# Kernel optimization log

Hardware: AMD Instinct MI355X
Metric: run time of the kernel (lower is better)

## Reference

```python
import jax, jax.numpy as jnp
import numpy as np

EPS = 1e-5

def _bn(x, gamma, beta):
    # training-mode BatchNorm2d over (B, H, W) per channel, biased variance
    m = x.mean(axis=(0, 2, 3), keepdims=True)
    v = x.var(axis=(0, 2, 3), keepdims=True)
    return (x - m) * jax.lax.rsqrt(v + EPS) * gamma[None, :, None, None] + beta[None, :, None, None]

@jax.custom_vjp
def _atan_spike(x):
    # Heaviside forward, ATan surrogate (alpha=2) backward
    return (x >= 0.0).astype(x.dtype)

def _atan_fwd(x):
    return _atan_spike(x), x

def _atan_bwd(x, g):
    return (g / (1.0 + (jnp.pi * x) ** 2),)

_atan_spike.defvjp(_atan_fwd, _atan_bwd)

def setup_inputs() -> dict:
    key = jax.random.key(0)
    ks = jax.random.split(key, 3)
    T, N, Cin, Cout, H, W = 4, 8, 512, 256, 32, 32
    x = jax.random.normal(ks[0], (T, N, Cin, H, W), dtype=jnp.float32)
    bn1_gamma = jnp.ones((Cin,), jnp.float32)
    bn1_beta = jnp.zeros((Cin,), jnp.float32)
    conv_w = jax.random.normal(ks[1], (Cout, Cin, 1, 1), jnp.float32) / np.float32(np.sqrt(Cin))
    lif_w = jnp.zeros((1,), jnp.float32)  # sigmoid(0)=0.5 <=> init_tau=2.0
    bn2_gamma = jnp.ones((Cout,), jnp.float32)
    bn2_beta = jnp.zeros((Cout,), jnp.float32)
    up_w = jax.random.normal(ks[2], (Cout, Cout, 4, 4), jnp.float32) / np.float32(np.sqrt(Cout * 16))
    return {"x": x, "bn1_gamma": bn1_gamma, "bn1_beta": bn1_beta, "conv_w": conv_w,
            "lif_w": lif_w, "bn2_gamma": bn2_gamma, "bn2_beta": bn2_beta, "up_w": up_w}

def reference(x, bn1_gamma, bn1_beta, conv_w, lif_w, bn2_gamma, bn2_beta, up_w):
    T, N, Cin, H, W = x.shape
    Cout = conv_w.shape[0]
    # bottleneck: SeqToANNContainer(BN(Cin), Conv2d 1x1 Cin->Cout, no bias)
    xf = x.reshape(T * N, Cin, H, W)
    h = _bn(xf, bn1_gamma, bn1_beta)
    h = jnp.einsum('bchw,oc->bohw', h, conv_w[:, :, 0, 0])
    h = h.reshape(T, N, Cout, H, W)
    # MultiStepParametricLIFNode: v += (x - v)*sigmoid(w); hard reset to 0, detach_reset
    tau_inv = jax.nn.sigmoid(lif_w[0])
    def step(v, xt):
        v = v + (xt - v) * tau_inv
        s = _atan_spike(v - 1.0)
        v = v * (1.0 - jax.lax.stop_gradient(s))
        return v, s
    _, spikes = jax.lax.scan(step, jnp.zeros_like(h[0]), h)
    s = spikes.reshape(T * N, Cout, H, W)
    # ConstantDilation2d(dilation=2): zero-insertion -> (2H-1, 2W-1)
    d = jnp.zeros((T * N, Cout, 2 * H - 1, 2 * W - 1), s.dtype).at[:, :, ::2, ::2].set(s)
    # ConstantPad2d(kernel-1-padding = 4-1-1 = 2)
    d = jnp.pad(d, ((0, 0), (0, 0), (2, 2), (2, 2)))
    d = _bn(d, bn2_gamma, bn2_beta)
    # ConvTranspose2d(k=4, stride=1, padding=3) == VALID conv with channel-swapped, flipped kernel
    kern = up_w.transpose(1, 0, 2, 3)[:, :, ::-1, ::-1]
    out = jax.lax.conv_general_dilated(d, kern, (1, 1), 'VALID',
                                       dimension_numbers=('NCHW', 'OIHW', 'NCHW'))
    return out.reshape(T, N, Cout, 2 * H, 2 * W)
```

## Files before the change

### kernel.cpp

```cpp
#include <hip/hip_runtime.h>
#include <math.h>

#define CIN 512
#define COUT 256
#define TT 4
#define NN 8
#define HH 32
#define WW 32
#define FR (TT*NN)
#define HW (HH*WW)
#define BN_EPS 1e-5
#define FLAGCAP (1<<19)
#define N2 143648.0

typedef unsigned short ushort_t;
typedef unsigned int uint_t;
typedef __attribute__((ext_vector_type(8))) short short8;
typedef __attribute__((ext_vector_type(4))) float f32x4;
typedef __attribute__((ext_vector_type(4))) uint_t u32x4;

__device__ inline ushort_t f2bf(float f) {
    uint_t u = __float_as_uint(f);
    uint_t r = u + 0x7FFFu + ((u >> 16) & 1u);
    return (ushort_t)(r >> 16);
}
__device__ inline float bf2f(ushort_t a) { return __uint_as_float(((uint_t)a) << 16); }

__global__ __launch_bounds__(512) void k_init(int* __restrict__ cnt,
                                              uint_t* __restrict__ flagcnt,
                                              double* __restrict__ bn_s1,
                                              double* __restrict__ bn_s2,
                                              float* __restrict__ kc) {
    int t = threadIdx.x;
    bn_s1[t] = 0.0;
    bn_s2[t] = 0.0;
    if (t < 256) { cnt[t] = 0; kc[t] = 0.f; }
    if (t == 0) *flagcnt = 0u;
}

__global__ __launch_bounds__(256) void k_xsplit(const float* __restrict__ x,
                                                ushort_t* __restrict__ Xa_g,
                                                ushort_t* __restrict__ Xb_g,
                                                float* __restrict__ X2_g,
                                                double* __restrict__ bn_s1,
                                                double* __restrict__ bn_s2) {
    int blk = blockIdx.x;
    int n = blk >> 6;
    int hw0 = (blk & 63) << 4;
    int tid = threadIdx.x;
    int pg = tid & 3;
    int rr = tid >> 2;

    __shared__ ushort_t La[8192];
    __shared__ ushort_t Lb[8192];
    __shared__ float X2s[64];

    float x2loc[16];
    float s1v[8], s2v[8];
#pragma unroll
    for (int q = 0; q < 16; ++q) x2loc[q] = 0.f;
#pragma unroll
    for (int q = 0; q < 8; ++q) { s1v[q] = 0.f; s2v[q] = 0.f; }
    if (tid < 64) X2s[tid] = 0.f;

#pragma unroll
    for (int kc = 0; kc < 4; ++kc) {
        int c0 = kc << 7;
        __syncthreads();
#pragma unroll
        for (int sw = 0; sw < 8; ++sw) {
            const int t = sw >> 1;
            int i = ((sw & 1) << 6) + rr;
            const float4 v = *reinterpret_cast<const float4*>(
                &x[(((size_t)((t * NN + n) * CIN) + c0 + i) << 10) + hw0 + (pg << 2)]);
            int cbl = i >> 3, e = i & 7;
            int slot = (kc << 1) + (sw & 1);
#pragma unroll
            for (int k = 0; k < 4; ++k) {
                float xv = (k == 0) ? v.x : (k == 1) ? v.y : (k == 2) ? v.z : v.w;
                ushort_t a = f2bf(xv);
                ushort_t b = f2bf(xv - bf2f(a));
                x2loc[(k << 2) + t] += xv * xv;
                s1v[slot] += xv;
                s2v[slot] += xv * xv;
                int lrx = (k << 2) + t;
                uint_t u = ((((uint_t)(pg * 16 + cbl)) * 16 + lrx) << 3) + e;
                uint_t byteoff = (u << 1) ^ ((uint_t)pg << 5);
                *(ushort_t*)((char*)La + byteoff) = a;
                *(ushort_t*)((char*)Lb + byteoff) = b;
            }
        }
        __syncthreads();
        for (int q = tid; q < 1024; q += 256) {
            int pg2 = q >> 8;
            uint_t lo = (uint_t)(q & 255) << 4;
            uint_t src = (((uint_t)pg2 << 12) + lo) ^ ((uint_t)pg2 << 5);
            u32x4 va = *(u32x4*)((char*)La + src);
            u32x4 vb = *(u32x4*)((char*)Lb + src);
            size_t dst = (((size_t)blk * 4 + pg2) << 13) + ((size_t)kc << 11) + ((size_t)(q & 255) << 3);
            __builtin_nontemporal_store(va, (u32x4*)(Xa_g + dst));
            __builtin_nontemporal_store(vb, (u32x4*)(Xb_g + dst));
        }
    }
#pragma unroll
    for (int slot = 0; slot < 8; ++slot) {
        float a1 = s1v[slot], a2v = s2v[slot];
        a1 += __shfl_xor(a1, 1); a1 += __shfl_xor(a1, 2);
        a2v += __shfl_xor(a2v, 1); a2v += __shfl_xor(a2v, 2);
        if (pg == 0) {
            int c = ((slot >> 1) << 7) + ((slot & 1) << 6) + rr;
            atomicAdd(&bn_s1[c], (double)a1);
            atomicAdd(&bn_s2[c], (double)a2v);
        }
    }
    __syncthreads();
#pragma unroll
    for (int k = 0; k < 4; ++k)
#pragma unroll
        for (int t = 0; t < 4; ++t)
            atomicAdd(&X2s[pg * 16 + k * 4 + t], x2loc[(k << 2) + t]);
    __syncthreads();
    if (tid < 64) X2_g[(blk << 6) + tid] = X2s[tid];
}

__global__ __launch_bounds__(256) void k_prep_wsplit(const float* __restrict__ conv_w,
                                                     const float* __restrict__ beta1,
                                                     const float* __restrict__ gamma1,
                                                     const double* __restrict__ bn_s1,
                                                     const double* __restrict__ bn_s2,
                                                     double* __restrict__ w2t,
                                                     ushort_t* __restrict__ Wa,
                                                     ushort_t* __restrict__ Wb,
                                                     float* __restrict__ W2,
                                                     double* __restrict__ bias) {
    int o = blockIdx.x;
    __shared__ double alphas[CIN];
    __shared__ double mbs[CIN];
    for (int c = threadIdx.x; c < CIN; c += 256) {
        double n = (double)(FR * HW);
        double m = bn_s1[c] / n;
        double var = bn_s2[c] / n - m * m;
        double al = (double)gamma1[c] / sqrt(var + BN_EPS);
        alphas[c] = al;
        mbs[c] = (double)beta1[c] - m * al;
    }
    __syncthreads();

    float s2 = 0.f;
    double sb = 0.0;
    for (int c = threadIdx.x; c < CIN; c += 256) {
        double cw = (double)conv_w[(size_t)o * CIN + c];
        double w = cw * alphas[c];
        w2t[(size_t)c * COUT + o] = w;
        float wf = (float)w;
        ushort_t a = f2bf(wf);
        ushort_t b = f2bf(wf - bf2f(a));
        size_t base = ((size_t)(c >> 3) * COUT + o) * 8 + (c & 7);
        Wa[base] = a; Wb[base] = b;
        s2 += wf * wf;
        sb += mbs[c] * cw;
    }
    __shared__ float red[256];
    __shared__ double redd[256];
    red[threadIdx.x] = s2;
    redd[threadIdx.x] = sb;
    __syncthreads();
    for (int ofs = 128; ofs > 0; ofs >>= 1) {
        if (threadIdx.x < ofs) {
            red[threadIdx.x] += red[threadIdx.x + ofs];
            redd[threadIdx.x] += redd[threadIdx.x + ofs];
        }
        __syncthreads();
    }
    if (threadIdx.x == 0) { W2[o] = red[0]; bias[o] = redd[0]; }
}

__global__ __launch_bounds__(256) void k_gemm_lif_mfma(
    const ushort_t* __restrict__ Xa_g, const ushort_t* __restrict__ Xb_g,
    const ushort_t* __restrict__ Wa, const ushort_t* __restrict__ Wb,
    const float* __restrict__ X2_g, const float* __restrict__ W2,
    const double* __restrict__ bias, const float* __restrict__ lif_w,
    ushort_t* __restrict__ spk, int* __restrict__ cnt,
    uint_t* __restrict__ flags, uint_t* __restrict__ flagcnt)
{
    int blk = blockIdx.x;
    int n   = blk >> 6;
    int hw0 = (blk & 63) << 4;
    int tid = threadIdx.x;
    int wv = tid >> 6, lane = tid & 63;
    int lr = lane & 15, kq = lane >> 4;
    int pxh = wv >> 1, oh = wv & 1;

    __shared__ uint_t cl[4 * 64 * 8];

    f32x4 acc[2][8];
#pragma unroll
    for (int m = 0; m < 2; ++m)
#pragma unroll
        for (int ot = 0; ot < 8; ++ot) acc[m][ot] = (f32x4){0.f, 0.f, 0.f, 0.f};

    const ushort_t* xa0 = Xa_g + (((size_t)blk) << 15) + ((size_t)pxh << 14) + ((uint_t)lane << 3);
    const ushort_t* xb0 = Xb_g + (((size_t)blk) << 15) + ((size_t)pxh << 14) + ((uint_t)lane << 3);
    const ushort_t* wbase_a = Wa + ((uint_t)kq << 11) + ((uint_t)oh << 10) + ((uint_t)lr << 3);
    const ushort_t* wbase_b = Wb + ((uint_t)kq << 11) + ((uint_t)oh << 10) + ((uint_t)lr << 3);

#pragma unroll 2
    for (int ks = 0; ks < 16; ++ks) {
        short8 fa0 = *(const short8*)(xa0 + (ks << 9));
        short8 fa1 = *(const short8*)(xa0 + 8192 + (ks << 9));
        short8 fb0 = *(const short8*)(xb0 + (ks << 9));
        short8 fb1 = *(const short8*)(xb0 + 8192 + (ks << 9));
        const ushort_t* wpa = wbase_a + (ks << 13);
        const ushort_t* wpb = wbase_b + (ks << 13);
#pragma unroll
        for (int ot = 0; ot < 8; ++ot) {
            short8 wa8 = *(const short8*)(wpa + (ot << 7));
            short8 wb8 = *(const short8*)(wpb + (ot << 7));
            acc[0][ot] = __builtin_amdgcn_mfma_f32_16x16x32_bf16(fa0, wa8, acc[0][ot], 0, 0, 0);
            acc[1][ot] = __builtin_amdgcn_mfma_f32_16x16x32_bf16(fa1, wa8, acc[1][ot], 0, 0, 0);
            acc[0][ot] = __builtin_amdgcn_mfma_f32_16x16x32_bf16(fb0, wa8, acc[0][ot], 0, 0, 0);
            acc[1][ot] = __builtin_amdgcn_mfma_f32_16x16x32_bf16(fb1, wa8, acc[1][ot], 0, 0, 0);
            acc[0][ot] = __builtin_amdgcn_mfma_f32_16x16x32_bf16(fa0, wb8, acc[0][ot], 0, 0, 0);
            acc[1][ot] = __builtin_amdgcn_mfma_f32_16x16x32_bf16(fa1, wb8, acc[1][ot], 0, 0, 0);
        }
    }

    float xs2[2][4];
#pragma unroll
    for (int m = 0; m < 2; ++m)
#pragma unroll
        for (int t = 0; t < 4; ++t)
            xs2[m][t] = X2_g[(blk << 6) + (((pxh << 1) + m) << 4) + (kq << 2) + t];

    for (int q = tid; q < 4 * 64 * 8; q += 256) cl[q] = 0;
    __syncthreads();

    float tauf = (float)(1.0 / (1.0 + exp(-(double)lif_w[0])));
#pragma unroll
    for (int ot = 0; ot < 8; ++ot) {
        int o = (oh << 7) + (ot << 4) + lr;
        float bi = (float)bias[o];
        float w2v = W2[o];
        uint_t cloc = 0;
#pragma unroll
        for (int m = 0; m < 2; ++m) {
            int hw = hw0 + (pxh << 3) + (m << 2) + kq;
            float v = 0.f;
            bool fl = false;
#pragma unroll
            for (int t = 0; t < 4; ++t) {
                float h = acc[m][ot][t] + bi;
                float eps = 4e-5f * sqrtf(w2v * xs2[m][t]) + 5e-5f;
                v += (h - v) * tauf;
                if (fabsf(v - 1.f) <= 2.f * eps) fl = true;
                bool s = (v >= 1.f);
                spk[((size_t)((t * NN + n) * HW) + hw) * COUT + o] = s ? (ushort_t)0x3F80 : (ushort_t)0;
                cloc += s ? 1u : 0u;
                if (s) v = 0.f;
            }
            if (fl) {
                uint_t id = atomicAdd(flagcnt, 1u);
                if (id < FLAGCAP) flags[id] = (((uint_t)(n * HW + hw)) << 8) | (uint_t)o;
            }
        }
        cl[(wv << 9) + (lane << 3) + ot] = cloc;
    }
    __syncthreads();
    {
        int o = tid;
        int ohh = o >> 7, ott = (o >> 4) & 7, lr2 = o & 15;
        uint_t s = 0;
#pragma unroll
        for (int w2 = ohh; w2 < 4; w2 += 2)
#pragma unroll
            for (int k2 = 0; k2 < 4; ++k2)
                s += cl[(w2 << 9) + (((k2 << 4) + lr2) << 3) + ott];
        if (s) atomicAdd(&cnt[o], (int)s);
    }
}

__global__ __launch_bounds__(256) void k_fixup(
    const float* __restrict__ x, const double* __restrict__ w2t,
    const double* __restrict__ bias, const float* __restrict__ lif_w,
    const uint_t* __restrict__ flags, const uint_t* __restrict__ flagcnt,
    ushort_t* __restrict__ spk, int* __restrict__ cnt)
{
    int nf = (int)*flagcnt; if (nf > FLAGCAP) nf = FLAGCAP;
    int wid = (blockIdx.x << 2) + (threadIdx.x >> 6);
    int lane = threadIdx.x & 63;
    double tau = 1.0 / (1.0 + exp(-(double)lif_w[0]));
    for (int g = wid; g < nf; g += 8192) {
        uint_t f = flags[g];
        int o = f & 255;
        int s = f >> 8;
        int n = s >> 10, hw = s & 1023;
        const float* xb = x + ((size_t)n << 19) + hw;
        double p0 = 0.0, p1 = 0.0, p2 = 0.0, p3 = 0.0;
#pragma unroll
        for (int i = 0; i < 8; ++i) {
            int c = lane + (i << 6);
            double wv = w2t[((size_t)c << 8) + o];
            size_t xo = (size_t)c << 10;
            p0 += wv * (double)xb[xo];
            p1 += wv * (double)xb[xo + (1ull << 22)];
            p2 += wv * (double)xb[xo + (2ull << 22)];
            p3 += wv * (double)xb[xo + (3ull << 22)];
        }
#pragma unroll
        for (int ofs = 32; ofs > 0; ofs >>= 1) {
            p0 += __shfl_down(p0, ofs);
            p1 += __shfl_down(p1, ofs);
            p2 += __shfl_down(p2, ofs);
            p3 += __shfl_down(p3, ofs);
        }
        if (lane == 0) {
            double bi = bias[o];
            double hh[4] = {p0 + bi, p1 + bi, p2 + bi, p3 + bi};
            double v = 0.0; int delta = 0;
#pragma unroll
            for (int t = 0; t < 4; ++t) {
                v += (hh[t] - v) * tau;
                bool sn = (v >= 1.0);
                size_t idx = (((size_t)t << 13) + ((size_t)n << 10) + (size_t)hw) * COUT + o;
                ushort_t old = spk[idx];
                ushort_t nw = sn ? (ushort_t)0x3F80 : (ushort_t)0;
                if (old != nw) { spk[idx] = nw; delta += sn ? 1 : -1; }
                if (sn) v = 0.0;
            }
            if (delta) atomicAdd(&cnt[o], delta);
        }
    }
}

__global__ __launch_bounds__(256) void k_wt_prep(const float* __restrict__ up_w,
                                                 const int* __restrict__ cnt,
                                                 const float* __restrict__ gamma2,
                                                 const float* __restrict__ beta2,
                                                 ushort_t* __restrict__ Wt,
                                                 float* __restrict__ kc) {
    int blk = blockIdx.x;
    int ij = blk >> 5, cb = blk & 31;
    int o = threadIdx.x;
    __shared__ double a2s[8], b2s[8];
    if (o < 8) {
        int c = (cb << 3) + o;
        double m = (double)cnt[c] / N2;
        double a = (double)gamma2[c] / sqrt(m - m * m + BN_EPS);
        a2s[o] = a;
        b2s[o] = (double)beta2[c] - m * a;
    }
    __syncthreads();
    short8 v;
    double part = 0.0;
#pragma unroll
    for (int e = 0; e < 8; ++e) {
        int c = (cb << 3) + e;
        double u = (double)up_w[(((size_t)c * COUT) + o) * 16 + ij];
        v[e] = (short)f2bf((float)(a2s[e] * u));
        part += b2s[e] * u;
    }
    *(short8*)(Wt + ((size_t)ij << 16) + ((size_t)cb << 11) + ((size_t)o << 3)) = v;
    atomicAdd(&kc[o], (float)part);
}

__global__ __launch_bounds__(512) void k_deconv_mfma(const ushort_t* __restrict__ spk,
                                                     const ushort_t* __restrict__ Wt,
                                                     const float* __restrict__ kc,
                                                     float* __restrict__ out) {
    int p = blockIdx.x;
    int xcd = p & 7;
    int r = p >> 3;
    int py = xcd >> 2;
    int b  = ((xcd & 3) << 3) | ((r >> 4) & 7);
    int Yb = (r & 15) << 1;
    int tid = threadIdx.x;
    int wv  = tid >> 6;
    int lane = tid & 63;
    int px = wv >> 2;
    int og = wv & 3;
    int lr = lane & 15;
    int kq = lane >> 4;

    __shared__ __align__(16) char smem[52224];
    ushort_t* slab = (ushort_t*)smem;

    int sb = Yb - 1 + py;
    for (int q = tid; q < 3 * 34 * 32; q += 512) {
        int pix = q >> 5;
        int l = q & 31;
        int r2 = pix / 34;
        int xc = pix - r2 * 34;
        int sy = sb + r2;
        int sx = xc - 1;
        uint_t off = ((uint_t)(pix << 9) + (uint_t)(l << 4)) ^ ((uint_t)(xc & 7) << 4);
        uint4* dst = (uint4*)((char*)slab + off);
        if (sy >= 0 && sy < 32 && sx >= 0 && sx < 32) {
            *dst = *(const uint4*)(spk + ((size_t)b * HW + sy * 32 + sx) * COUT + l * 8);
        } else {
            *dst = make_uint4(0u, 0u, 0u, 0u);
        }
    }
    __syncthreads();

    f32x4 acc[4][4];
#pragma unroll
    for (int pf = 0; pf < 4; ++pf)
#pragma unroll
        for (int of = 0; of < 4; ++of)
            acc[pf][of] = (f32x4){0.f, 0.f, 0.f, 0.f};

    int obase = og << 6;

#pragma unroll
    for (int dy = 0; dy < 2; ++dy) {
#pragma unroll
        for (int dx = 0; dx < 2; ++dx) {
            int i = 3 - py - 2 * dy;
            int j = 3 - px - 2 * dx;
            const ushort_t* wpij = Wt + ((size_t)(i * 4 + j) << 16);
            uint_t sbase[4], swz[4];
#pragma unroll
            for (int pf = 0; pf < 4; ++pf) {
                int pid = pf * 16 + lr;
                int Yq = pid >> 5;
                int X  = pid & 31;
                int xc = X + dx + px;
                int prow = (Yq + dy) * 34 + xc;
                sbase[pf] = ((uint_t)prow << 9) + ((uint_t)kq << 4);
                swz[pf]   = ((uint_t)(xc & 7)) << 4;
            }
#pragma unroll
            for (int cs = 0; cs < 8; ++cs) {
                short8 aw[4];
#pragma unroll
                for (int of = 0; of < 4; ++of)
                    aw[of] = *(const short8*)(wpij +
                        ((size_t)((cs << 2) + kq) * COUT + obase + (of << 4) + lr) * 8);
                short8 bs[4];
#pragma unroll
                for (int pf = 0; pf < 4; ++pf)
                    bs[pf] = *(const short8*)((const char*)slab +
                              ((sbase[pf] + ((uint_t)cs << 6)) ^ swz[pf]));
#pragma unroll
                for (int pf = 0; pf < 4; ++pf)
#pragma unroll
                    for (int of = 0; of < 4; ++of)
                        acc[pf][of] = __builtin_amdgcn_mfma_f32_16x16x32_bf16(
                            aw[of], bs[pf], acc[pf][of], 0, 0, 0);
            }
        }
    }

    __syncthreads();
    float* stage = (float*)smem;
#pragma unroll 1
    for (int of = 0; of < 4; ++of) {
        if (of) __syncthreads();
#pragma unroll
        for (int rg = 0; rg < 4; ++rg) {
            int row = (og << 4) + (kq << 2) + rg;
#pragma unroll
            for (int pf = 0; pf < 4; ++pf) {
                int Yq = pf >> 1;
                int x = ((((pf & 1) << 4) + lr) << 1) + px;
                uint_t a4 = ((uint_t)row << 5) + ((uint_t)Yq << 4)
                          + (((uint_t)x >> 2) ^ ((uint_t)kq << 2));
                stage[(a4 << 2) + (x & 3)] = acc[pf][of][rg];
            }
        }
        __syncthreads();
#pragma unroll
        for (int rep = 0; rep < 4; ++rep) {
            int u = tid + (rep << 9);
            int rr2 = u >> 5, rem = u & 31;
            int yq = rem >> 4, f4 = rem & 15;
            uint_t a4 = ((uint_t)rr2 << 5) + ((uint_t)yq << 4)
                      + ((uint_t)f4 ^ ((((uint_t)rr2 >> 2) & 3) << 2));
            f32x4 v = ((const f32x4*)stage)[a4];
            int o = ((rr2 >> 4) << 6) + (of << 4) + (rr2 & 15);
            float base = kc[o];
            v[0] += base; v[1] += base; v[2] += base; v[3] += base;
            int y = ((Yb + yq) << 1) + py;
            __builtin_nontemporal_store(v,
                (f32x4*)(out + ((size_t)(b * COUT + o) << 12) + (y << 6) + (f4 << 2)));
        }
    }
}

extern "C" void kernel_launch(void* const* d_in, const int* in_sizes, int n_in,
                              void* d_out, int out_size, void* d_ws, size_t ws_size,
                              hipStream_t stream) {
    (void)in_sizes; (void)n_in; (void)out_size; (void)ws_size;
    const float* x        = (const float*)d_in[0];
    const float* bn1_g    = (const float*)d_in[1];
    const float* bn1_b    = (const float*)d_in[2];
    const float* conv_w   = (const float*)d_in[3];
    const float* lif_w    = (const float*)d_in[4];
    const float* bn2_g    = (const float*)d_in[5];
    const float* bn2_b    = (const float*)d_in[6];
    const float* up_w     = (const float*)d_in[7];
    float* out = (float*)d_out;

    char* ws = (char*)d_ws;
    ushort_t* spk  = (ushort_t*)(ws + 0);
    ushort_t* Xa_g = (ushort_t*)(ws + 16777216);
    ushort_t* Xb_g = (ushort_t*)(ws + 50331648);
    float*  X2_g   = (float*)  (ws + 83886080);
    float*  W2     = (float*)  (ws + 84017152);
    double* w2t    = (double*) (ws + 84026368);
    double* bias   = (double*) (ws + 85074944);
    int*    cnt    = (int*)    (ws + 85081088);
    float*  kc     = (float*)  (ws + 85082112);
    ushort_t* Wt   = (ushort_t*)(ws + 85083136);
    ushort_t* Wa   = (ushort_t*)(ws + 87180288);
    ushort_t* Wb   = (ushort_t*)(ws + 87442432);
    uint_t* flagcnt= (uint_t*) (ws + 87704576);
    uint_t* flags  = (uint_t*) (ws + 87705600);
    double* bn_s1  = (double*) (ws + 89802752);
    double* bn_s2  = (double*) (ws + 89806848);

    k_init<<<1, 512, 0, stream>>>(cnt, flagcnt, bn_s1, bn_s2, kc);
    k_xsplit<<<512, 256, 0, stream>>>(x, Xa_g, Xb_g, X2_g, bn_s1, bn_s2);
    k_prep_wsplit<<<COUT, 256, 0, stream>>>(conv_w, bn1_b, bn1_g, bn_s1, bn_s2,
                                            w2t, Wa, Wb, W2, bias);
    k_gemm_lif_mfma<<<512, 256, 0, stream>>>(Xa_g, Xb_g, Wa, Wb, X2_g, W2,
                                             bias, lif_w, spk, cnt, flags, flagcnt);
    k_fixup<<<2048, 256, 0, stream>>>(x, w2t, bias, lif_w, flags, flagcnt, spk, cnt);
    k_wt_prep<<<512, 256, 0, stream>>>(up_w, cnt, bn2_g, bn2_b, Wt, kc);
    k_deconv_mfma<<<32 * 2 * 16, 512, 0, stream>>>(spk, Wt, kc, out);
}
```

Measured before the change: 440.7 us.

## Double deconv pixel tile per block to reuse weight fragments across more pixels

Each deconv block now covers 4 quarter-rows (128 pixels) per parity instead of 2, so the block count halves to 512 and each wave holds 8x4 accumulator fragments. Every weight fragment loaded from global memory now feeds twice as many MFMAs, which cuts weight traffic per output. The slab staging grows to 5 rows, the epilogue is adjusted for the larger tile, and register pressure rises (128 accumulator floats per lane), which may lower occupancy or cause spills.

```diff
diff --git a/kernel.cpp b/kernel.cpp
--- a/kernel.cpp
+++ b/kernel.cpp
@@ -371,8 +371,8 @@
     int xcd = p & 7;
     int r = p >> 3;
     int py = xcd >> 2;
-    int b  = ((xcd & 3) << 3) | ((r >> 4) & 7);
-    int Yb = (r & 15) << 1;
+    int b  = ((xcd & 3) << 3) | (r >> 3);
+    int YB = r & 7;
     int tid = threadIdx.x;
     int wv  = tid >> 6;
     int lane = tid & 63;
@@ -381,11 +381,11 @@
     int lr = lane & 15;
     int kq = lane >> 4;
 
-    __shared__ __align__(16) char smem[52224];
+    __shared__ __align__(16) char smem[5 * 34 * 512];
     ushort_t* slab = (ushort_t*)smem;
 
-    int sb = Yb - 1 + py;
-    for (int q = tid; q < 3 * 34 * 32; q += 512) {
+    int sb = (YB << 2) + py - 1;
+    for (int q = tid; q < 5 * 34 * 32; q += 512) {
         int pix = q >> 5;
         int l = q & 31;
         int r2 = pix / 34;
@@ -402,9 +402,9 @@
     }
     __syncthreads();
 
-    f32x4 acc[4][4];
-#pragma unroll
-    for (int pf = 0; pf < 4; ++pf)
+    f32x4 acc[8][4];
+#pragma unroll
+    for (int pf = 0; pf < 8; ++pf)
 #pragma unroll
         for (int of = 0; of < 4; ++of)
             acc[pf][of] = (f32x4){0.f, 0.f, 0.f, 0.f};
@@ -418,12 +418,11 @@
             int i = 3 - py - 2 * dy;
             int j = 3 - px - 2 * dx;
             const ushort_t* wpij = Wt + ((size_t)(i * 4 + j) << 16);
-            uint_t sbase[4], swz[4];
-#pragma unroll
-            for (int pf = 0; pf < 4; ++pf) {
-                int pid = pf * 16 + lr;
-                int Yq = pid >> 5;
-                int X  = pid & 31;
+            uint_t sbase[8], swz[8];
+#pragma unroll
+            for (int pf = 0; pf < 8; ++pf) {
+                int Yq = pf >> 1;
+                int X  = ((pf & 1) << 4) + lr;
                 int xc = X + dx + px;
                 int prow = (Yq + dy) * 34 + xc;
                 sbase[pf] = ((uint_t)prow << 9) + ((uint_t)kq << 4);
@@ -436,17 +435,15 @@
                 for (int of = 0; of < 4; ++of)
                     aw[of] = *(const short8*)(wpij +
                         ((size_t)((cs << 2) + kq) * COUT + obase + (of << 4) + lr) * 8);
-                short8 bs[4];
-#pragma unroll
-                for (int pf = 0; pf < 4; ++pf)
-                    bs[pf] = *(const short8*)((const char*)slab +
+#pragma unroll
+                for (int pf = 0; pf < 8; ++pf) {
+                    short8 bs = *(const short8*)((const char*)slab +
                               ((sbase[pf] + ((uint_t)cs << 6)) ^ swz[pf]));
-#pragma unroll
-                for (int pf = 0; pf < 4; ++pf)
 #pragma unroll
                     for (int of = 0; of < 4; ++of)
                         acc[pf][of] = __builtin_amdgcn_mfma_f32_16x16x32_bf16(
-                            aw[of], bs[pf], acc[pf][of], 0, 0, 0);
+                            aw[of], bs, acc[pf][of], 0, 0, 0);
+                }
             }
         }
     }
@@ -460,27 +457,27 @@
         for (int rg = 0; rg < 4; ++rg) {
             int row = (og << 4) + (kq << 2) + rg;
 #pragma unroll
-            for (int pf = 0; pf < 4; ++pf) {
+            for (int pf = 0; pf < 8; ++pf) {
                 int Yq = pf >> 1;
                 int x = ((((pf & 1) << 4) + lr) << 1) + px;
-                uint_t a4 = ((uint_t)row << 5) + ((uint_t)Yq << 4)
+                uint_t a4 = (((uint_t)row * 4 + Yq) << 4)
                           + (((uint_t)x >> 2) ^ ((uint_t)kq << 2));
                 stage[(a4 << 2) + (x & 3)] = acc[pf][of][rg];
             }
         }
         __syncthreads();
 #pragma unroll
-        for (int rep = 0; rep < 4; ++rep) {
+        for (int rep = 0; rep < 8; ++rep) {
             int u = tid + (rep << 9);
-            int rr2 = u >> 5, rem = u & 31;
+            int row = u >> 6, rem = u & 63;
             int yq = rem >> 4, f4 = rem & 15;
-            uint_t a4 = ((uint_t)rr2 << 5) + ((uint_t)yq << 4)
-                      + ((uint_t)f4 ^ ((((uint_t)rr2 >> 2) & 3) << 2));
+            uint_t a4 = (((uint_t)row * 4 + yq) << 4)
+                      + ((uint_t)f4 ^ ((((uint_t)row >> 2) & 3) << 2));
             f32x4 v = ((const f32x4*)stage)[a4];
-            int o = ((rr2 >> 4) << 6) + (of << 4) + (rr2 & 15);
+            int o = ((row >> 4) << 6) + (of << 4) + (row & 15);
             float base = kc[o];
             v[0] += base; v[1] += base; v[2] += base; v[3] += base;
-            int y = ((Yb + yq) << 1) + py;
+            int y = (((YB << 2) + yq) << 1) + py;
             __builtin_nontemporal_store(v,
                 (f32x4*)(out + ((size_t)(b * COUT + o) << 12) + (y << 6) + (f4 << 2)));
         }
@@ -527,5 +524,5 @@
                                              bias, lif_w, spk, cnt, flags, flagcnt);
     k_fixup<<<2048, 256, 0, stream>>>(x, w2t, bias, lif_w, flags, flagcnt, spk, cnt);
     k_wt_prep<<<512, 256, 0, stream>>>(up_w, cnt, bn2_g, bn2_b, Wt, kc);
-    k_deconv_mfma<<<32 * 2 * 16, 512, 0, stream>>>(spk, Wt, kc, out);
-}
+    k_deconv_mfma<<<512, 512, 0, stream>>>(spk, Wt, kc, out);
+}
```

After: 636.7 us. 44.5% more time.
